# Optimization experiments

Hardware: AMD Instinct MI355X
Metric: run time of the kernel (lower is better)

The kernel has to match this reference:

```python
import jax, jax.numpy as jnp
import numpy as np
from jax import lax

NUM_HEADS = 16
PADDING_L = 15


def setup_inputs() -> dict:
    key = jax.random.key(0)
    k1, k2 = jax.random.split(key)
    T, B, C = 2048, 8, 1024
    H, K = NUM_HEADS, 31
    x = jax.random.normal(k1, (T, B, C), dtype=jnp.float32)
    weight = jax.random.normal(k2, (H, 1, K), dtype=jnp.float32)
    bias = jnp.zeros((C,), dtype=jnp.float32)
    return {"x": x, "weight": weight, "bias": bias}


def reference(x, weight, bias):
    # x: (T, B, C); weight: (H, 1, K); bias: (C,)
    T, B, C = x.shape
    H, _, K = weight.shape
    R = C // H  # channels per head sharing one kernel
    # weight_softmax=True: normalize kernel taps per head
    w = jax.nn.softmax(weight.reshape(H, K), axis=-1)
    # Expand the shared per-head kernel to one kernel per channel (depthwise conv)
    w_full = jnp.repeat(w, R, axis=0).reshape(C, 1, K)  # (C, 1, K) = OIH
    xb = jnp.transpose(x, (1, 2, 0))  # (B, C, T) = NCH
    # Depthwise correlation: y[t] = sum_k w[k] * x[t + k - padding_l]
    y = lax.conv_general_dilated(
        xb, w_full,
        window_strides=(1,),
        padding=[(PADDING_L, K - 1 - PADDING_L)],
        feature_group_count=C,
        dimension_numbers=("NCH", "OIH", "NCH"),
    )  # (B, C, T)
    out = jnp.transpose(y, (2, 0, 1))  # back to (T, B, C)
    return out + bias.reshape(1, 1, -1)
```

## Files before the change

kernel.cpp:

```cpp
#include <hip/hip_runtime.h>
#include <utility>
#include <cmath>

constexpr int T = 2048;
constexpr int B = 8;
constexpr int C = 1024;
constexpr int H = 16;
constexpr int K = 31;
constexpr int PAD = 15;
constexpr int NBC = B * C;
constexpr int BLOCK = 256;
constexpr int TT = 32;
constexpr int WIN = TT + K - 1;

template <int KK>
__device__ __forceinline__ void tap(float (&acc)[TT], const float (&xv)[WIN], float wk) {
#pragma unroll
    for (int i = 0; i < TT; ++i)
        acc[i] = fmaf(wk, xv[i + KK], acc[i]);
}

template <int... Ks>
__device__ __forceinline__ void all_taps(float (&acc)[TT], const float (&xv)[WIN],
                                         const float (&w)[K],
                                         std::integer_sequence<int, Ks...>) {
    (tap<Ks>(acc, xv, w[Ks]), ...);
}

template <int... Ks>
__device__ __forceinline__ void bcast_taps(float (&w)[K], float v,
                                           std::integer_sequence<int, Ks...>) {
    ((w[Ks] = __int_as_float(__builtin_amdgcn_readlane(__float_as_int(v), Ks))), ...);
}

__global__ __launch_bounds__(BLOCK, 4) void lconv_tbc_kernel(
    const float* __restrict__ x,
    const float* __restrict__ wgt,
    const float* __restrict__ bias,
    float* __restrict__ out)
{
    const int tid  = threadIdx.x;
    const int lane = tid & 63;
    const int bc   = blockIdx.x * BLOCK + tid;
    const int c    = bc & (C - 1);
    const int t0   = blockIdx.y * TT;
    const int tstart = t0 - PAD;

    const int head = c >> 6;
    float raw = (lane < K) ? wgt[head * K + lane] : -INFINITY;
    float m = raw;
    #pragma unroll
    for (int off = 32; off >= 1; off >>= 1) m = fmaxf(m, __shfl_xor(m, off));
    float e = (lane < K) ? expf(raw - m) : 0.0f;
    float s = e;
    #pragma unroll
    for (int off = 32; off >= 1; off >>= 1) s += __shfl_xor(s, off);
    const float myw = e / s;

    float w[K];
    bcast_taps(w, myw, std::make_integer_sequence<int, K>{});

    float xv[WIN];
    if (tstart >= 0 && tstart + WIN <= T) {
        const float* rowp = x + (size_t)tstart * NBC;
        #pragma unroll
        for (int j = 0; j < WIN; ++j)
            xv[j] = rowp[(size_t)j * NBC + bc];
    } else {
        #pragma unroll
        for (int j = 0; j < WIN; ++j) {
            const int tg = tstart + j;
            xv[j] = ((unsigned)tg < (unsigned)T) ? x[(size_t)tg * NBC + bc] : 0.0f;
        }
    }

    __builtin_amdgcn_sched_barrier(0);

    float acc[TT];
    #pragma unroll
    for (int i = 0; i < TT; ++i) acc[i] = 0.0f;
    all_taps(acc, xv, w, std::make_integer_sequence<int, K>{});

    const float bb = bias[c];
    float* op = out + (size_t)t0 * NBC + bc;
    #pragma unroll
    for (int i = 0; i < TT; ++i)
        __builtin_nontemporal_store(acc[i] + bb, &op[(size_t)i * NBC]);
}

extern "C" void kernel_launch(void* const* d_in, const int* in_sizes, int n_in,
                              void* d_out, int out_size, void* d_ws, size_t ws_size,
                              hipStream_t stream) {
    const float* x    = (const float*)d_in[0];
    const float* wgt  = (const float*)d_in[1];
    const float* bias = (const float*)d_in[2];
    float* out        = (float*)d_out;

    dim3 grid(NBC / BLOCK, T / TT);
    lconv_tbc_kernel<<<grid, dim3(BLOCK), 0, stream>>>(x, wgt, bias, out);
}
```

Measured before the change: 31.67 us.

## Process four time tiles per block with register sliding window and prefetch

```diff
diff --git a/kernel.cpp b/kernel.cpp
--- a/kernel.cpp
+++ b/kernel.cpp
@@ -12,6 +12,7 @@
 constexpr int BLOCK = 256;
 constexpr int TT = 32;
 constexpr int WIN = TT + K - 1;
+constexpr int TILES = 4;
 
 template <int KK>
 __device__ __forceinline__ void tap(float (&acc)[TT], const float (&xv)[WIN], float wk) {
@@ -33,7 +34,7 @@
     ((w[Ks] = __int_as_float(__builtin_amdgcn_readlane(__float_as_int(v), Ks))), ...);
 }
 
-__global__ __launch_bounds__(BLOCK, 4) void lconv_tbc_kernel(
+__global__ __launch_bounds__(BLOCK, 3) void lconv_tbc_kernel(
     const float* __restrict__ x,
     const float* __restrict__ wgt,
     const float* __restrict__ bias,
@@ -43,8 +44,7 @@
     const int lane = tid & 63;
     const int bc   = blockIdx.x * BLOCK + tid;
     const int c    = bc & (C - 1);
-    const int t0   = blockIdx.y * TT;
-    const int tstart = t0 - PAD;
+    const int t0   = blockIdx.y * (TILES * TT);
 
     const int head = c >> 6;
     float raw = (lane < K) ? wgt[head * K + lane] : -INFINITY;
@@ -59,33 +59,46 @@
 
     float w[K];
     bcast_taps(w, myw, std::make_integer_sequence<int, K>{});
+    const float bb = bias[c];
 
     float xv[WIN];
-    if (tstart >= 0 && tstart + WIN <= T) {
-        const float* rowp = x + (size_t)tstart * NBC;
+    #pragma unroll
+    for (int j = 0; j < WIN; ++j) {
+        const int tg = t0 - PAD + j;
+        xv[j] = ((unsigned)tg < (unsigned)T)
+                  ? x[(ptrdiff_t)tg * NBC + bc] : 0.0f;
+    }
+
+    float xn[TT];
+    #pragma unroll 1
+    for (int it = 0; it < TILES; ++it) {
+        if (it + 1 < TILES) {
+            const int tn0 = t0 + (WIN - PAD) + it * TT;
+            #pragma unroll
+            for (int j = 0; j < TT; ++j) {
+                const int tg = tn0 + j;
+                xn[j] = (tg < T) ? x[(ptrdiff_t)tg * NBC + bc] : 0.0f;
+            }
+        }
+        __builtin_amdgcn_sched_barrier(0);
+
+        float acc[TT];
         #pragma unroll
-        for (int j = 0; j < WIN; ++j)
-            xv[j] = rowp[(size_t)j * NBC + bc];
-    } else {
+        for (int i = 0; i < TT; ++i) acc[i] = 0.0f;
+        all_taps(acc, xv, w, std::make_integer_sequence<int, K>{});
+
+        float* op = out + (size_t)(t0 + it * TT) * NBC + bc;
         #pragma unroll
-        for (int j = 0; j < WIN; ++j) {
-            const int tg = tstart + j;
-            xv[j] = ((unsigned)tg < (unsigned)T) ? x[(size_t)tg * NBC + bc] : 0.0f;
+        for (int i = 0; i < TT; ++i)
+            __builtin_nontemporal_store(acc[i] + bb, &op[(size_t)i * NBC]);
+
+        if (it + 1 < TILES) {
+            #pragma unroll
+            for (int j = 0; j < WIN - TT; ++j) xv[j] = xv[j + TT];
+            #pragma unroll
+            for (int j = 0; j < TT; ++j)       xv[WIN - TT + j] = xn[j];
         }
     }
-
-    __builtin_amdgcn_sched_barrier(0);
-
-    float acc[TT];
-    #pragma unroll
-    for (int i = 0; i < TT; ++i) acc[i] = 0.0f;
-    all_taps(acc, xv, w, std::make_integer_sequence<int, K>{});
-
-    const float bb = bias[c];
-    float* op = out + (size_t)t0 * NBC + bc;
-    #pragma unroll
-    for (int i = 0; i < TT; ++i)
-        __builtin_nontemporal_store(acc[i] + bb, &op[(size_t)i * NBC]);
 }
 
 extern "C" void kernel_launch(void* const* d_in, const int* in_sizes, int n_in,
@@ -96,6 +109,6 @@
     const float* bias = (const float*)d_in[2];
     float* out        = (float*)d_out;
 
-    dim3 grid(NBC / BLOCK, T / TT);
+    dim3 grid(NBC / BLOCK, T / (TILES * TT));
     lconv_tbc_kernel<<<grid, dim3(BLOCK), 0, stream>>>(x, wgt, bias, out);
 }
```

Result: slower. 33.96 us (+7.3%).

## Stage input window through LDS with direct global-to-LDS 128-bit loads

Applied to the files above, without the earlier changes.

```diff
diff --git a/kernel.cpp b/kernel.cpp
--- a/kernel.cpp
+++ b/kernel.cpp
@@ -9,9 +9,11 @@
 constexpr int K = 31;
 constexpr int PAD = 15;
 constexpr int NBC = B * C;
-constexpr int BLOCK = 256;
+constexpr int BLOCK = 64;
 constexpr int TT = 32;
 constexpr int WIN = TT + K - 1;
+constexpr int ROWSP = 64;
+constexpr int NG = ROWSP / 4;
 
 template <int KK>
 __device__ __forceinline__ void tap(float (&acc)[TT], const float (&xv)[WIN], float wk) {
@@ -33,18 +35,40 @@
     ((w[Ks] = __int_as_float(__builtin_amdgcn_readlane(__float_as_int(v), Ks))), ...);
 }
 
+__device__ __forceinline__ void gld_lds_b128(const float* gsrc, float* ldst) {
+    __builtin_amdgcn_global_load_lds(
+        (const __attribute__((address_space(1))) unsigned int*)gsrc,
+        (__attribute__((address_space(3))) unsigned int*)ldst,
+        16, 0, 0);
+}
+
 __global__ __launch_bounds__(BLOCK, 4) void lconv_tbc_kernel(
     const float* __restrict__ x,
     const float* __restrict__ wgt,
     const float* __restrict__ bias,
+    const float* __restrict__ zbuf,
     float* __restrict__ out)
 {
-    const int tid  = threadIdx.x;
-    const int lane = tid & 63;
-    const int bc   = blockIdx.x * BLOCK + tid;
-    const int c    = bc & (C - 1);
+    __shared__ float xs[ROWSP * BLOCK];
+
+    const int lane = threadIdx.x;
+    const int bc0  = blockIdx.x * BLOCK;
+    const int c    = (bc0 + lane) & (C - 1);
     const int t0   = blockIdx.y * TT;
     const int tstart = t0 - PAD;
+
+    const int lane_row = lane >> 4;
+    const int lane_col = (lane & 15) * 4;
+    const ptrdiff_t lane_off = (ptrdiff_t)lane_row * NBC + lane_col;
+    const float* zsrc = zbuf + lane_col;
+    #pragma unroll
+    for (int g = 0; g < NG; ++g) {
+        const int tg0 = tstart + 4 * g;
+        const int tg  = tg0 + lane_row;
+        const float* src = x + (ptrdiff_t)tg0 * NBC + bc0 + lane_off;
+        const float* p   = ((unsigned)tg < (unsigned)T) ? src : zsrc;
+        gld_lds_b128(p, &xs[g * 4 * BLOCK]);
+    }
 
     const int head = c >> 6;
     float raw = (lane < K) ? wgt[head * K + lane] : -INFINITY;
@@ -59,30 +83,22 @@
 
     float w[K];
     bcast_taps(w, myw, std::make_integer_sequence<int, K>{});
+    const float bb = bias[c];
+
+    asm volatile("s_waitcnt vmcnt(0)" ::: "memory");
+    __builtin_amdgcn_sched_barrier(0);
 
     float xv[WIN];
-    if (tstart >= 0 && tstart + WIN <= T) {
-        const float* rowp = x + (size_t)tstart * NBC;
-        #pragma unroll
-        for (int j = 0; j < WIN; ++j)
-            xv[j] = rowp[(size_t)j * NBC + bc];
-    } else {
-        #pragma unroll
-        for (int j = 0; j < WIN; ++j) {
-            const int tg = tstart + j;
-            xv[j] = ((unsigned)tg < (unsigned)T) ? x[(size_t)tg * NBC + bc] : 0.0f;
-        }
-    }
-
-    __builtin_amdgcn_sched_barrier(0);
+    #pragma unroll
+    for (int j = 0; j < WIN; ++j)
+        xv[j] = xs[j * BLOCK + lane];
 
     float acc[TT];
     #pragma unroll
     for (int i = 0; i < TT; ++i) acc[i] = 0.0f;
     all_taps(acc, xv, w, std::make_integer_sequence<int, K>{});
 
-    const float bb = bias[c];
-    float* op = out + (size_t)t0 * NBC + bc;
+    float* op = out + (size_t)t0 * NBC + bc0 + lane;
     #pragma unroll
     for (int i = 0; i < TT; ++i)
         __builtin_nontemporal_store(acc[i] + bb, &op[(size_t)i * NBC]);
@@ -95,7 +111,10 @@
     const float* wgt  = (const float*)d_in[1];
     const float* bias = (const float*)d_in[2];
     float* out        = (float*)d_out;
+    float* zbuf       = (float*)d_ws;
+
+    hipMemsetAsync(zbuf, 0, 256, stream);
 
     dim3 grid(NBC / BLOCK, T / TT);
-    lconv_tbc_kernel<<<grid, dim3(BLOCK), 0, stream>>>(x, wgt, bias, out);
+    lconv_tbc_kernel<<<grid, dim3(BLOCK), 0, stream>>>(x, wgt, bias, zbuf, out);
 }
```

New measurement: 40.24 us. 1.27x slower.

## Split softmax into prekernel and use 2-channel vector tiles with shorter time strips

Applied to the files above, without the earlier changes.

```diff
diff --git a/kernel.cpp b/kernel.cpp
--- a/kernel.cpp
+++ b/kernel.cpp
@@ -3,89 +3,108 @@
 #include <cmath>
 
 constexpr int T = 2048;
-constexpr int B = 8;
 constexpr int C = 1024;
-constexpr int H = 16;
 constexpr int K = 31;
 constexpr int PAD = 15;
-constexpr int NBC = B * C;
+constexpr int NBC = 8192;
 constexpr int BLOCK = 256;
-constexpr int TT = 32;
-constexpr int WIN = TT + K - 1;
+constexpr int TPT = 16;
+constexpr int WIN = TPT + K - 1;
+constexpr int CPB = 64;
+constexpr int TRB = 128;
+
+typedef __attribute__((ext_vector_type(2))) float f32x2;
+
+__device__ __forceinline__ f32x2 aload2(const float* p) {
+    f32x2 r;
+    asm volatile("global_load_dwordx2 %0, %1, off" : "=v"(r) : "v"(p));
+    return r;
+}
 
 template <int KK>
-__device__ __forceinline__ void tap(float (&acc)[TT], const float (&xv)[WIN], float wk) {
+__device__ __forceinline__ void tap(f32x2 (&acc)[TPT], const f32x2 (&xv)[WIN], float wk) {
 #pragma unroll
-    for (int i = 0; i < TT; ++i)
-        acc[i] = fmaf(wk, xv[i + KK], acc[i]);
+    for (int i = 0; i < TPT; ++i) {
+        acc[i].x = fmaf(wk, xv[i + KK].x, acc[i].x);
+        acc[i].y = fmaf(wk, xv[i + KK].y, acc[i].y);
+    }
 }
-
 template <int... Ks>
-__device__ __forceinline__ void all_taps(float (&acc)[TT], const float (&xv)[WIN],
+__device__ __forceinline__ void all_taps(f32x2 (&acc)[TPT], const f32x2 (&xv)[WIN],
                                          const float (&w)[K],
                                          std::integer_sequence<int, Ks...>) {
     (tap<Ks>(acc, xv, w[Ks]), ...);
 }
 
-template <int... Ks>
-__device__ __forceinline__ void bcast_taps(float (&w)[K], float v,
-                                           std::integer_sequence<int, Ks...>) {
-    ((w[Ks] = __int_as_float(__builtin_amdgcn_readlane(__float_as_int(v), Ks))), ...);
+__global__ __launch_bounds__(64) void softmax_w_kernel(const float* __restrict__ wgt,
+                                                       float* __restrict__ wtab) {
+    const int head = blockIdx.x;
+    const int lane = threadIdx.x;
+    float raw = (lane < K) ? wgt[head * K + lane] : -INFINITY;
+    float m = raw;
+#pragma unroll
+    for (int off = 32; off >= 1; off >>= 1) m = fmaxf(m, __shfl_xor(m, off));
+    float e = (lane < K) ? expf(raw - m) : 0.0f;
+    float s = e;
+#pragma unroll
+    for (int off = 32; off >= 1; off >>= 1) s += __shfl_xor(s, off);
+    if (lane < 32) wtab[head * 32 + lane] = (lane < K) ? e / s : 0.0f;
 }
 
-__global__ __launch_bounds__(BLOCK, 4) void lconv_tbc_kernel(
+__global__ __launch_bounds__(BLOCK, 3) void lconv_main(
     const float* __restrict__ x,
-    const float* __restrict__ wgt,
     const float* __restrict__ bias,
+    const float* __restrict__ wtab,
+    const float* __restrict__ zbuf,
     float* __restrict__ out)
 {
     const int tid  = threadIdx.x;
-    const int lane = tid & 63;
-    const int bc   = blockIdx.x * BLOCK + tid;
-    const int c    = bc & (C - 1);
-    const int t0   = blockIdx.y * TT;
+    const int cx   = tid & 31;
+    const int ty   = tid >> 5;
+    const int bc0  = blockIdx.x * CPB;
+    const int c0   = bc0 & (C - 1);
+    const int head = c0 >> 6;
+    const int t0   = blockIdx.y * TRB + ty * TPT;
     const int tstart = t0 - PAD;
 
-    const int head = c >> 6;
-    float raw = (lane < K) ? wgt[head * K + lane] : -INFINITY;
-    float m = raw;
-    #pragma unroll
-    for (int off = 32; off >= 1; off >>= 1) m = fmaxf(m, __shfl_xor(m, off));
-    float e = (lane < K) ? expf(raw - m) : 0.0f;
-    float s = e;
-    #pragma unroll
-    for (int off = 32; off >= 1; off >>= 1) s += __shfl_xor(s, off);
-    const float myw = e / s;
+    float w[K];
+    const float* wp = wtab + head * 32;
+#pragma unroll
+    for (int k = 0; k < K; ++k) w[k] = wp[k];
 
-    float w[K];
-    bcast_taps(w, myw, std::make_integer_sequence<int, K>{});
+    const f32x2 bias2 = *(const f32x2*)(bias + c0 + 2 * cx);
 
-    float xv[WIN];
-    if (tstart >= 0 && tstart + WIN <= T) {
-        const float* rowp = x + (size_t)tstart * NBC;
-        #pragma unroll
+    f32x2 xv[WIN];
+    const float* base = x + (ptrdiff_t)tstart * NBC + bc0 + 2 * cx;
+    if (blockIdx.y >= 1 && blockIdx.y <= 14) {
+#pragma unroll
         for (int j = 0; j < WIN; ++j)
-            xv[j] = rowp[(size_t)j * NBC + bc];
+            xv[j] = aload2(base + (ptrdiff_t)j * NBC);
     } else {
-        #pragma unroll
+        const float* zsrc = zbuf + 2 * cx;
+#pragma unroll
         for (int j = 0; j < WIN; ++j) {
             const int tg = tstart + j;
-            xv[j] = ((unsigned)tg < (unsigned)T) ? x[(size_t)tg * NBC + bc] : 0.0f;
+            const float* p = ((unsigned)tg < (unsigned)T)
+                               ? (base + (ptrdiff_t)j * NBC) : zsrc;
+            xv[j] = aload2(p);
         }
     }
 
+    asm volatile("s_waitcnt vmcnt(0)" ::: "memory");
     __builtin_amdgcn_sched_barrier(0);
 
-    float acc[TT];
-    #pragma unroll
-    for (int i = 0; i < TT; ++i) acc[i] = 0.0f;
+    f32x2 acc[TPT];
+#pragma unroll
+    for (int i = 0; i < TPT; ++i) acc[i] = f32x2{0.0f, 0.0f};
     all_taps(acc, xv, w, std::make_integer_sequence<int, K>{});
 
-    const float bb = bias[c];
-    float* op = out + (size_t)t0 * NBC + bc;
-    #pragma unroll
-    for (int i = 0; i < TT; ++i)
-        __builtin_nontemporal_store(acc[i] + bb, &op[(size_t)i * NBC]);
+    float* op = out + (ptrdiff_t)t0 * NBC + bc0 + 2 * cx;
+#pragma unroll
+    for (int i = 0; i < TPT; ++i) {
+        const f32x2 v = acc[i] + bias2;
+        __builtin_nontemporal_store(v, (f32x2*)(op + (ptrdiff_t)i * NBC));
+    }
 }
 
 extern "C" void kernel_launch(void* const* d_in, const int* in_sizes, int n_in,
@@ -95,7 +114,12 @@
     const float* wgt  = (const float*)d_in[1];
     const float* bias = (const float*)d_in[2];
     float* out        = (float*)d_out;
+    float* wtab       = (float*)d_ws;
+    const float* zbuf = (const float*)d_ws + 512;
 
-    dim3 grid(NBC / BLOCK, T / TT);
-    lconv_tbc_kernel<<<grid, dim3(BLOCK), 0, stream>>>(x, wgt, bias, out);
+    hipMemsetAsync(d_ws, 0, 8192, stream);
+    softmax_w_kernel<<<dim3(16), dim3(64), 0, stream>>>(wgt, wtab);
+
+    dim3 grid(NBC / CPB, T / TRB);
+    lconv_main<<<grid, dim3(BLOCK), 0, stream>>>(x, bias, wtab, zbuf, out);
 }
```

Measured after the change: 35.24 us. +11.3%, slower.
